# Optimization experiments

Measured on AMD Instinct MI355X. Metric: run time of the kernel, lower is better.

Reference implementation:

```python
import jax, jax.numpy as jnp
import numpy as np

V, E, D, H = 50000, 800000, 128, 128  # nodes, edges, node_feat_size, graph_feat_size
NEG_SLOPE = 0.01  # nn.LeakyReLU default


def setup_inputs() -> dict:
    key = jax.random.key(0)
    ks = jax.random.split(key, 11)
    s = 0.05
    return {
        "node_feats": jax.random.normal(ks[0], (V, D), jnp.float32),
        "W_edge": jax.random.normal(ks[1], (1, 2 * D), jnp.float32) * s,
        "b_edge": jnp.zeros((1,), jnp.float32),
        "W_proj": jax.random.normal(ks[2], (H, D), jnp.float32) * s,
        "b_proj": jnp.zeros((H,), jnp.float32),
        "W_ih": jax.random.normal(ks[3], (3 * D, H), jnp.float32) * s,
        "W_hh": jax.random.normal(ks[4], (3 * D, D), jnp.float32) * s,
        "b_ih": jnp.zeros((3 * D,), jnp.float32),
        "b_hh": jnp.zeros((3 * D,), jnp.float32),
        "src": jax.random.randint(ks[5], (E,), 0, V),
        "dst": jax.random.randint(ks[6], (E,), 0, V),
    }


def _leaky_relu(x):
    return jnp.where(x >= 0, x, NEG_SLOPE * x)


def _edge_softmax(logits, dst, num_nodes):
    # segment softmax over edges grouped by destination node; logits: [E, 1]
    m = jax.ops.segment_max(logits, dst, num_segments=num_nodes)
    m = jnp.where(jnp.isfinite(m), m, 0.0)  # guard empty segments
    e = jnp.exp(logits - m[dst])
    s = jax.ops.segment_sum(e, dst, num_segments=num_nodes)
    return e / s[dst]


def reference(node_feats, W_edge, b_edge, W_proj, b_proj, W_ih, W_hh, b_ih, b_hh, src, dst):
    # GNNLayer.apply_edges: he = cat([dst_feat, src_feat])  [E, 2D]
    he = jnp.concatenate([node_feats[dst], node_feats[src]], axis=1)
    # project_edge: Dropout (eval: identity) -> Linear(2D, 1) -> LeakyReLU
    logits = _leaky_relu(he @ W_edge.T + b_edge)  # [E, 1]
    # AttentiveGRU2: edge_softmax per dst
    a = _edge_softmax(logits, dst, V)  # [E, 1]
    # project_node: Dropout (eval) -> Linear(D, H)
    hv = node_feats @ W_proj.T + b_proj  # [V, H]
    # src_mul_edge + sum aggregation to dst
    m = hv[src] * a  # [E, H]
    c = jax.ops.segment_sum(m, dst, num_segments=V)  # [V, H]
    context = jax.nn.elu(c)
    # PyTorch GRUCell(context, node_feats)
    gi = context @ W_ih.T + b_ih      # [V, 3D]
    gh = node_feats @ W_hh.T + b_hh   # [V, 3D]
    i_r, i_z, i_n = jnp.split(gi, 3, axis=1)
    h_r, h_z, h_n = jnp.split(gh, 3, axis=1)
    r = jax.nn.sigmoid(i_r + h_r)
    z = jax.nn.sigmoid(i_z + h_z)
    n = jnp.tanh(i_n + r * h_n)
    h_new = (1.0 - z) * n + z * node_feats
    return jax.nn.relu(h_new)
```

## Files before the change

### kernel.cpp

```cpp
#include <hip/hip_runtime.h>
#include <hip/hip_bf16.h>


#define V_NODES 50000
#define E_EDGES 800000
#define D_FEAT  128
#define GCHUNK  5
#define WS_BLOCKS 1250
#define GRU_BLOCKS 1264

#define NCHUNK  49
#define CHUNK_E 16384
#define RANGES  4
#define NODE_R  12500
#define HISTG   (NCHUNK * RANGES)
#define SCAN_BLOCKS 196

typedef short bf16x8 __attribute__((ext_vector_type(8)));
typedef float f32x4  __attribute__((ext_vector_type(4)));
typedef unsigned short u16x4 __attribute__((ext_vector_type(4)));

#define OFF_WEDGE 0
#define OFF_WPROJ 256
#define OFF_WIH   16640
#define OFF_WHH   65792
#define OFF_BEDGE 114944
#define OFF_BPROJ 114945
#define OFF_BIH   115073
#define OFF_BHH   115457
#define SMALL_TOTAL 115841
#define CONV_X_BLOCKS   6250
#define CONV_S_BLOCKS   453
#define HIST_BLOCKS     3125

__device__ int   g_is_bf16;
__device__ float g_pd[V_NODES];
__device__ float g_ps[V_NODES];
__device__ __attribute__((aligned(16))) unsigned int g_mat[NCHUNK * V_NODES];
__device__ int   g_row_off[V_NODES + 1];
__device__ int   g_blocksum[SCAN_BLOCKS];
__device__ unsigned short g_rank16[E_EDGES];
__device__ __attribute__((aligned(16))) int2 g_s_pair[E_EDGES];
__device__ __attribute__((aligned(16))) unsigned short g_xbf[V_NODES * D_FEAT];
__device__ __attribute__((aligned(16))) unsigned short g_wsmall[SMALL_TOTAL + 15];
__device__ __attribute__((aligned(16))) unsigned short g_hv[V_NODES * D_FEAT];
__device__ __attribute__((aligned(16))) unsigned short g_ctx[V_NODES * D_FEAT];

static __device__ __forceinline__ float b2f(unsigned short u) {
  union { unsigned int i; float f; } v; v.i = ((unsigned int)u) << 16; return v.f;
}
static __device__ __forceinline__ unsigned short f2b(float f) {
  unsigned int i = __float_as_uint(f);
  unsigned int r = (i + 0x7FFFu + ((i >> 16) & 1u)) >> 16;
  return (unsigned short)r;
}
static __device__ __forceinline__ bf16x8 load_frag(const unsigned short* p) {
  return *reinterpret_cast<const bf16x8*>(p);
}
static __device__ __forceinline__ float fast_rcp(float x) {
  return __builtin_amdgcn_rcpf(x);
}
static __device__ __forceinline__ float fast_sigmoid(float x) {
  return fast_rcp(1.f + __expf(-x));
}
static __device__ __forceinline__ float fast_tanh(float y) {
  return 1.f - 2.f * fast_rcp(__expf(2.f * y) + 1.f);
}

__global__ void probe_kernel(const unsigned int* __restrict__ x)
{
  __shared__ int cnt;
  if (threadIdx.x == 0) cnt = 0;
  __syncthreads();
  const unsigned int w  = x[threadIdx.x];
  const unsigned int lo = w & 0xFFFFu;
  const unsigned int ex = (lo >> 7) & 0xFFu;
  if (lo != 0u && ex >= 118u && ex <= 132u) atomicAdd(&cnt, 1);
  __syncthreads();
  if (threadIdx.x == 0) g_is_bf16 = (cnt >= 200) ? 1 : 0;
}

__global__ void conv_fused_kernel(
    const void* __restrict__ x,
    const void* p0, const void* p1, const void* p2, const void* p3,
    const void* p4, const void* p5, const void* p6, const void* p7)
{
  const int b = blockIdx.x;
  if (b < CONV_X_BLOCKS) {
    const int t = b * 256 + threadIdx.x;
    if (g_is_bf16) {
      reinterpret_cast<u16x4*>(g_xbf)[t] = reinterpret_cast<const u16x4*>(x)[t];
    } else {
      const float4 v = reinterpret_cast<const float4*>(x)[t];
      u16x4 o; o.x = f2b(v.x); o.y = f2b(v.y); o.z = f2b(v.z); o.w = f2b(v.w);
      reinterpret_cast<u16x4*>(g_xbf)[t] = o;
    }
  } else {
    const int i = (b - CONV_X_BLOCKS) * 256 + threadIdx.x;
    if (i >= SMALL_TOTAL) return;
    const int offs[9] = {OFF_WEDGE, OFF_WPROJ, OFF_WIH, OFF_WHH,
                         OFF_BEDGE, OFF_BPROJ, OFF_BIH, OFF_BHH, SMALL_TOTAL};
    const void* ps[8] = {p0, p1, p2, p3, p4, p5, p6, p7};
    int r = 0;
#pragma unroll
    for (int k = 0; k < 8; k++) if (i >= offs[k]) r = k;
    const int j = i - offs[r];
    g_wsmall[i] = g_is_bf16
        ? reinterpret_cast<const unsigned short*>(ps[r])[j]
        : f2b(reinterpret_cast<const float*>(ps[r])[j]);
  }
}

__global__ __launch_bounds__(256, 2) void np_hist_kernel(const int* __restrict__ dst)
{
  __shared__ unsigned int hloc[NODE_R / 2];
  const int b = blockIdx.x;
  if (b < HISTG) {
    const int c  = b >> 2;
    const int r0 = (b & 3) * NODE_R;
    for (int i = threadIdx.x; i < NODE_R / 2; i += 256) hloc[i] = 0u;
    __syncthreads();
    const int ebase = c * CHUNK_E;
    const int ecnt  = min(CHUNK_E, E_EDGES - ebase);
    const int4* dst4 = reinterpret_cast<const int4*>(dst + ebase);
    const int n4 = ecnt >> 2;
    for (int i = threadIdx.x; i < n4; i += 256) {
      const int4 d4 = dst4[i];
      const int e0 = ebase + (i << 2);
      const unsigned int rx = (unsigned int)(d4.x - r0);
      const unsigned int ry = (unsigned int)(d4.y - r0);
      const unsigned int rz = (unsigned int)(d4.z - r0);
      const unsigned int rw = (unsigned int)(d4.w - r0);
      if (rx < (unsigned int)NODE_R) {
        const unsigned int sh = (rx & 1u) << 4;
        const unsigned int old = atomicAdd(&hloc[rx >> 1], 1u << sh);
        g_rank16[e0] = (unsigned short)((old >> sh) & 0xFFFFu);
      }
      if (ry < (unsigned int)NODE_R) {
        const unsigned int sh = (ry & 1u) << 4;
        const unsigned int old = atomicAdd(&hloc[ry >> 1], 1u << sh);
        g_rank16[e0 + 1] = (unsigned short)((old >> sh) & 0xFFFFu);
      }
      if (rz < (unsigned int)NODE_R) {
        const unsigned int sh = (rz & 1u) << 4;
        const unsigned int old = atomicAdd(&hloc[rz >> 1], 1u << sh);
        g_rank16[e0 + 2] = (unsigned short)((old >> sh) & 0xFFFFu);
      }
      if (rw < (unsigned int)NODE_R) {
        const unsigned int sh = (rw & 1u) << 4;
        const unsigned int old = atomicAdd(&hloc[rw >> 1], 1u << sh);
        g_rank16[e0 + 3] = (unsigned short)((old >> sh) & 0xFFFFu);
      }
    }
    __syncthreads();
    uint2* mout = reinterpret_cast<uint2*>(&g_mat[c * V_NODES + r0]);
    for (int i = threadIdx.x; i < NODE_R / 2; i += 256) {
      const unsigned int w = hloc[i];
      mout[i] = make_uint2(w & 0xFFFFu, w >> 16);
    }
    return;
  }
  const int g     = (b - HISTG) * 4 + (threadIdx.x >> 6);
  const int lane  = threadIdx.x & 63;
  const int cg    = g & 7;
  const int chunk = g >> 3;
  const int col   = lane & 15;
  const int quad  = lane >> 4;
  const int h     = 16 * cg + col;

  bf16x8 bw[4];
#pragma unroll
  for (int kk = 0; kk < 4; kk++)
    bw[kk] = load_frag(g_wsmall + OFF_WPROJ + h * D_FEAT + kk * 32 + quad * 8);
  bf16x8 be[4];
#pragma unroll
  for (int kk = 0; kk < 4; kk++) { be[kk] = bf16x8{0,0,0,0,0,0,0,0}; }
  if (cg == 0 && col < 2) {
#pragma unroll
    for (int kk = 0; kk < 4; kk++)
      be[kk] = load_frag(g_wsmall + OFF_WEDGE + col * D_FEAT + kk * 32 + quad * 8);
  }
  const float bp = b2f(g_wsmall[OFF_BPROJ + h]);

  const int t0 = chunk * GCHUNK;
  bf16x8 a[4];
#pragma unroll
  for (int kk = 0; kk < 4; kk++)
    a[kk] = load_frag(g_xbf + (t0 * 16 + col) * D_FEAT + kk * 32 + quad * 8);
  for (int t = t0; t < t0 + GCHUNK; t++) {
    const int tn = (t + 1 < t0 + GCHUNK) ? t + 1 : t;
    bf16x8 na[4];
#pragma unroll
    for (int kk = 0; kk < 4; kk++)
      na[kk] = load_frag(g_xbf + (tn * 16 + col) * D_FEAT + kk * 32 + quad * 8);
    f32x4 acc; acc[0]=0.f; acc[1]=0.f; acc[2]=0.f; acc[3]=0.f;
#pragma unroll
    for (int kk = 0; kk < 4; kk++)
      acc = __builtin_amdgcn_mfma_f32_16x16x32_bf16(a[kk], bw[kk], acc, 0, 0, 0);
#pragma unroll
    for (int r = 0; r < 4; r++)
      g_hv[(t * 16 + quad * 4 + r) * D_FEAT + h] = f2b(acc[r] + bp);
    if (cg == 0) {
      f32x4 acce; acce[0]=0.f; acce[1]=0.f; acce[2]=0.f; acce[3]=0.f;
#pragma unroll
      for (int kk = 0; kk < 4; kk++)
        acce = __builtin_amdgcn_mfma_f32_16x16x32_bf16(a[kk], be[kk], acce, 0, 0, 0);
      if (col == 0) {
#pragma unroll
        for (int r = 0; r < 4; r++) g_pd[t * 16 + quad * 4 + r] = acce[r];
      } else if (col == 1) {
#pragma unroll
        for (int r = 0; r < 4; r++) g_ps[t * 16 + quad * 4 + r] = acce[r];
      }
    }
#pragma unroll
    for (int kk = 0; kk < 4; kk++) a[kk] = na[kk];
  }
}

__global__ __launch_bounds__(256) void scan_a_kernel()
{
  __shared__ int lds[256];
  const int b = blockIdx.x, t = threadIdx.x;
  const int idx = b * 256 + t;
  int v = 0;
  if (idx < V_NODES) {
#pragma unroll 7
    for (int c = 0; c < NCHUNK; c++) v += (int)g_mat[c * V_NODES + idx];
  }
  lds[t] = v;
  __syncthreads();
  for (int off = 1; off < 256; off <<= 1) {
    int tmp = (t >= off) ? lds[t - off] : 0;
    __syncthreads();
    lds[t] += tmp;
    __syncthreads();
  }
  if (idx < V_NODES) g_row_off[idx] = lds[t] - v;
  if (t == 255) g_blocksum[b] = lds[255];
}

__global__ __launch_bounds__(256) void scan_bcm_kernel()
{
  __shared__ int lds[256];
  const int b = blockIdx.x, t = threadIdx.x;
  const int v = (t < SCAN_BLOCKS) ? g_blocksum[t] : 0;
  lds[t] = v;
  __syncthreads();
  for (int off = 1; off < 256; off <<= 1) {
    int tmp = (t >= off) ? lds[t - off] : 0;
    __syncthreads();
    lds[t] += tmp;
    __syncthreads();
  }
  const int total = lds[255];
  const int boff  = (b == 0) ? 0 : lds[b - 1];
  const int idx = b * 256 + t;
  if (idx < V_NODES) {
    int running = g_row_off[idx] + boff;
    g_row_off[idx] = running;
#pragma unroll 7
    for (int c = 0; c < NCHUNK; c++) {
      const unsigned int cnt = g_mat[c * V_NODES + idx];
      g_mat[c * V_NODES + idx] = (unsigned int)running;
      running += (int)cnt;
    }
  }
  if (b == 0 && t == 0) g_row_off[V_NODES] = total;
}

__global__ void edge_scatter_kernel(
    const int* __restrict__ src, const int* __restrict__ dst, int E)
{
  int e = blockIdx.x * blockDim.x + threadIdx.x;
  if (e >= E) return;
  const int d = dst[e], sn = src[e];
  float logit = g_pd[d] + g_ps[sn] + b2f(g_wsmall[OFF_BEDGE]);
  logit = (logit >= 0.f) ? logit : 0.01f * logit;
  const float w = __expf(logit);
  const int c = e >> 14;
  const int pos = (int)g_mat[c * V_NODES + d] + (int)g_rank16[e];
  g_s_pair[pos] = make_int2(sn, __float_as_int(w));
}

__global__ __launch_bounds__(256) void aggregate_kernel()
{
  const int v = blockIdx.x * 4 + (threadIdx.x >> 6);
  const int lane = threadIdx.x & 63;
  const int beg = g_row_off[v], end = g_row_off[v + 1];
  float accx = 0.f, accy = 0.f, ssum = 0.f;
  int i = beg;
  for (; i + 4 <= end; i += 4) {
    const int2 q0 = g_s_pair[i],     q1 = g_s_pair[i + 1],
               q2 = g_s_pair[i + 2], q3 = g_s_pair[i + 3];
    const float w0 = __int_as_float(q0.y), w1 = __int_as_float(q1.y),
                w2 = __int_as_float(q2.y), w3 = __int_as_float(q3.y);
    const unsigned int p0 = *reinterpret_cast<const unsigned int*>(g_hv + q0.x * D_FEAT + lane * 2);
    const unsigned int p1 = *reinterpret_cast<const unsigned int*>(g_hv + q1.x * D_FEAT + lane * 2);
    const unsigned int p2 = *reinterpret_cast<const unsigned int*>(g_hv + q2.x * D_FEAT + lane * 2);
    const unsigned int p3 = *reinterpret_cast<const unsigned int*>(g_hv + q3.x * D_FEAT + lane * 2);
    ssum += (w0 + w1) + (w2 + w3);
    accx += w0 * b2f((unsigned short)(p0 & 0xFFFFu)) + w1 * b2f((unsigned short)(p1 & 0xFFFFu))
          + w2 * b2f((unsigned short)(p2 & 0xFFFFu)) + w3 * b2f((unsigned short)(p3 & 0xFFFFu));
    accy += w0 * b2f((unsigned short)(p0 >> 16)) + w1 * b2f((unsigned short)(p1 >> 16))
          + w2 * b2f((unsigned short)(p2 >> 16)) + w3 * b2f((unsigned short)(p3 >> 16));
  }
  for (; i < end; i++) {
    const int2 q = g_s_pair[i];
    const float w = __int_as_float(q.y);
    ssum += w;
    const unsigned int pair =
        *reinterpret_cast<const unsigned int*>(g_hv + q.x * D_FEAT + lane * 2);
    accx += w * b2f((unsigned short)(pair & 0xFFFFu));
    accy += w * b2f((unsigned short)(pair >> 16));
  }
  const float inv = (end > beg) ? (1.0f / ssum) : 0.0f;
  float c0 = accx * inv, c1 = accy * inv;
  c0 = (c0 > 0.f) ? c0 : (__expf(c0) - 1.f);
  c1 = (c1 > 0.f) ? c1 : (__expf(c1) - 1.f);
  const unsigned int outp = ((unsigned int)f2b(c1) << 16) | (unsigned int)f2b(c0);
  *reinterpret_cast<unsigned int*>(g_ctx + v * D_FEAT + lane * 2) = outp;
}

__global__ __launch_bounds__(256, 2) void gru_kernel(const float* __restrict__ xf32,
                                                     float* __restrict__ out)
{
  const int d = blockIdx.x;
  const int x = d & 7;
  const int s = d >> 3;
  const int chunk = x + 8 * (s >> 1);
  if (chunk >= 625) return;
  const int half  = s & 1;
  const int wid   = threadIdx.x >> 6;
  const int lane  = threadIdx.x & 63;
  const int cg    = half * 4 + wid;
  const int col   = lane & 15;
  const int quad  = lane >> 4;
  const int h     = 16 * cg + col;
  const unsigned short* W_ih = g_wsmall + OFF_WIH;
  const unsigned short* W_hh = g_wsmall + OFF_WHH;
  const int isb = g_is_bf16;

  const float br  = b2f(g_wsmall[OFF_BIH + h])       + b2f(g_wsmall[OFF_BHH + h]);
  const float bz  = b2f(g_wsmall[OFF_BIH + 128 + h]) + b2f(g_wsmall[OFF_BHH + 128 + h]);
  const float bn  = b2f(g_wsmall[OFF_BIH + 256 + h]);
  const float bh_ = b2f(g_wsmall[OFF_BHH + 256 + h]);

  bf16x8 bIHr[4], bHHr[4], bIHz[4], bHHz[4], bIHn[4], bHHn[4];
#pragma unroll
  for (int kk = 0; kk < 4; kk++) {
    const int ko = kk * 32 + quad * 8;
    bIHr[kk] = load_frag(W_ih + h * D_FEAT + ko);
    bHHr[kk] = load_frag(W_hh + h * D_FEAT + ko);
    bIHz[kk] = load_frag(W_ih + (128 + h) * D_FEAT + ko);
    bHHz[kk] = load_frag(W_hh + (128 + h) * D_FEAT + ko);
    bIHn[kk] = load_frag(W_ih + (256 + h) * D_FEAT + ko);
    bHHn[kk] = load_frag(W_hh + (256 + h) * D_FEAT + ko);
  }

  const int t0 = chunk * GCHUNK;
  for (int t = t0; t < t0 + GCHUNK; t++) {
    const int arow = t * 16 + col;
    bf16x8 ax[4], ac[4];
#pragma unroll
    for (int kk = 0; kk < 4; kk++) {
      const int o = arow * D_FEAT + kk * 32 + quad * 8;
      ax[kk] = load_frag(g_xbf + o);
      ac[kk] = load_frag(g_ctx + o);
    }
    float xv[4];
    if (isb) {
#pragma unroll
      for (int r = 0; r < 4; r++)
        xv[r] = b2f(g_xbf[(t * 16 + quad * 4 + r) * D_FEAT + h]);
    } else {
#pragma unroll
      for (int r = 0; r < 4; r++)
        xv[r] = xf32[(t * 16 + quad * 4 + r) * D_FEAT + h];
    }
    f32x4 racc, zacc, niacc, nhacc;
    racc[0]=br;  racc[1]=br;  racc[2]=br;  racc[3]=br;
    zacc[0]=bz;  zacc[1]=bz;  zacc[2]=bz;  zacc[3]=bz;
    niacc[0]=bn; niacc[1]=bn; niacc[2]=bn; niacc[3]=bn;
    nhacc[0]=bh_; nhacc[1]=bh_; nhacc[2]=bh_; nhacc[3]=bh_;
#pragma unroll
    for (int kk = 0; kk < 4; kk++) {
      racc  = __builtin_amdgcn_mfma_f32_16x16x32_bf16(ac[kk], bIHr[kk], racc, 0, 0, 0);
      racc  = __builtin_amdgcn_mfma_f32_16x16x32_bf16(ax[kk], bHHr[kk], racc, 0, 0, 0);
      zacc  = __builtin_amdgcn_mfma_f32_16x16x32_bf16(ac[kk], bIHz[kk], zacc, 0, 0, 0);
      zacc  = __builtin_amdgcn_mfma_f32_16x16x32_bf16(ax[kk], bHHz[kk], zacc, 0, 0, 0);
      niacc = __builtin_amdgcn_mfma_f32_16x16x32_bf16(ac[kk], bIHn[kk], niacc, 0, 0, 0);
      nhacc = __builtin_amdgcn_mfma_f32_16x16x32_bf16(ax[kk], bHHn[kk], nhacc, 0, 0, 0);
    }
#pragma unroll
    for (int r = 0; r < 4; r++) {
      const int vrow = t * 16 + quad * 4 + r;
      const float rg = fast_sigmoid(racc[r]);
      const float zg = fast_sigmoid(zacc[r]);
      const float n  = fast_tanh(niacc[r] + rg * nhacc[r]);
      const float hn = (1.f - zg) * n + zg * xv[r];
      out[vrow * D_FEAT + h] = (hn < 0.f) ? 0.f : hn;
    }
  }
}

extern "C" void kernel_launch(void* const* d_in, const int* in_sizes, int n_in,
                              void* d_out, int out_size, void* d_ws, size_t ws_size,
                              hipStream_t stream)
{
  (void)d_ws; (void)ws_size; (void)out_size;

  int ix = -1, iWe = -1, ibe = -1, iWp = -1, ibp = -1,
      iWih = -1, iWhh = -1, ibih = -1, ibhh = -1, isrc = -1, idst = -1;
  for (int i = 0; i < n_in; i++) {
    const int s = in_sizes[i];
    if      (s == 6400000) ix = i;
    else if (s == 256)     iWe = i;
    else if (s == 1)       ibe = i;
    else if (s == 16384)   iWp = i;
    else if (s == 128)     ibp = i;
    else if (s == 49152)   { if (iWih < 0) iWih = i; else iWhh = i; }
    else if (s == 384)     { if (ibih < 0) ibih = i; else ibhh = i; }
    else if (s == 800000)  { if (isrc < 0) isrc = i; else idst = i; }
  }
  if (ix < 0 || iWe < 0 || ibe < 0 || iWp < 0 || ibp < 0 || iWih < 0 ||
      iWhh < 0 || ibih < 0 || ibhh < 0 || isrc < 0 || idst < 0) {
    ix = 0; iWe = 1; ibe = 2; iWp = 3; ibp = 4;
    iWih = 5; iWhh = 6; ibih = 7; ibhh = 8; isrc = 9; idst = 10;
  }

  const int* src = (const int*)d_in[isrc];
  const int* dst = (const int*)d_in[idst];
  float* out = (float*)d_out;

  probe_kernel<<<1, 256, 0, stream>>>((const unsigned int*)d_in[ix]);
  conv_fused_kernel<<<CONV_X_BLOCKS + CONV_S_BLOCKS, 256, 0, stream>>>(
      d_in[ix],
      d_in[iWe], d_in[iWp], d_in[iWih], d_in[iWhh],
      d_in[ibe], d_in[ibp], d_in[ibih], d_in[ibhh]);
  np_hist_kernel<<<HISTG + WS_BLOCKS, 256, 0, stream>>>(dst);
  scan_a_kernel<<<SCAN_BLOCKS, 256, 0, stream>>>();
  scan_bcm_kernel<<<SCAN_BLOCKS, 256, 0, stream>>>();
  edge_scatter_kernel<<<HIST_BLOCKS, 256, 0, stream>>>(src, dst, E_EDGES);
  aggregate_kernel<<<V_NODES / 4, 256, 0, stream>>>();
  gru_kernel<<<GRU_BLOCKS, 256, 0, stream>>>((const float*)d_in[ix], out);
}
```

Before: 233.9 us.

## Double-buffer GRU A-tiles in LDS via async global-to-LDS loads

The GRU kernel now stages each 16-row tile of x and context into a double-buffered, XOR-swizzled LDS buffer using global_load_lds async copies, and prefetches the next tile while computing the current one. Each wave then reads its MFMA A fragments from LDS instead of issuing strided global loads. The aim is to hide global memory latency and coalesce the tile fetch. The cost is LDS use and a __syncthreads per iteration. There is also a correctness risk, since no explicit vmcnt wait is visible before the LDS reads and the swizzle mapping has to be consistent between writer and reader.

```diff
diff --git a/kernel.cpp b/kernel.cpp
--- a/kernel.cpp
+++ b/kernel.cpp
@@ -65,6 +65,11 @@
 }
 static __device__ __forceinline__ float fast_tanh(float y) {
   return 1.f - 2.f * fast_rcp(__expf(2.f * y) + 1.f);
+}
+static __device__ __forceinline__ void async_copy16(const void* g, void* l) {
+  __builtin_amdgcn_global_load_lds(
+      (const __attribute__((address_space(1))) void*)g,
+      (__attribute__((address_space(3))) void*)l, 16, 0, 0);
 }
 
 __global__ void probe_kernel(const unsigned int* __restrict__ x)
@@ -330,6 +335,7 @@
   const int s = d >> 3;
   const int chunk = x + 8 * (s >> 1);
   if (chunk >= 625) return;
+  __shared__ __attribute__((aligned(16))) char lds_s[2][8192];
   const int half  = s & 1;
   const int wid   = threadIdx.x >> 6;
   const int lane  = threadIdx.x & 63;
@@ -358,15 +364,31 @@
     bHHn[kk] = load_frag(W_hh + (256 + h) * D_FEAT + ko);
   }
 
+  const int o_lin = wid * 1024 + lane * 16;
+  const int o_src = o_lin ^ (((o_lin >> 8) & 7) << 4);
+  const char* xbf_b = reinterpret_cast<const char*>(g_xbf);
+  const char* ctx_b = reinterpret_cast<const char*>(g_ctx);
+
   const int t0 = chunk * GCHUNK;
-  for (int t = t0; t < t0 + GCHUNK; t++) {
-    const int arow = t * 16 + col;
+  async_copy16(xbf_b + (size_t)t0 * 4096 + o_src, &lds_s[0][wid * 1024]);
+  async_copy16(ctx_b + (size_t)t0 * 4096 + o_src, &lds_s[0][4096 + wid * 1024]);
+
+  for (int i = 0; i < GCHUNK; i++) {
+    const int t = t0 + i;
+    const int buf = i & 1;
+    __syncthreads();
     bf16x8 ax[4], ac[4];
 #pragma unroll
     for (int kk = 0; kk < 4; kk++) {
-      const int o = arow * D_FEAT + kk * 32 + quad * 8;
-      ax[kk] = load_frag(g_xbf + o);
-      ac[kk] = load_frag(g_ctx + o);
+      const int phys = (col * 256 + kk * 64 + quad * 16) ^ ((col & 7) << 4);
+      ax[kk] = *reinterpret_cast<const bf16x8*>(&lds_s[buf][phys]);
+      ac[kk] = *reinterpret_cast<const bf16x8*>(&lds_s[buf][4096 + phys]);
+    }
+    if (i + 1 < GCHUNK) {
+      async_copy16(xbf_b + (size_t)(t + 1) * 4096 + o_src,
+                   &lds_s[buf ^ 1][wid * 1024]);
+      async_copy16(ctx_b + (size_t)(t + 1) * 4096 + o_src,
+                   &lds_s[buf ^ 1][4096 + wid * 1024]);
     }
     float xv[4];
     if (isb) {
```

Result: faster. 222.0 us (-5.1%).
